# Kernel tuning notes

Measured on AMD Instinct MI355X. Metric: run time of the kernel, lower is better.

The kernel has to match this reference:

```python
import jax, jax.numpy as jnp
import numpy as np

K = 32        # num_classes
NQ = 16384    # num query samples
C = 512       # feature_dim
H_REF = 512   # refinement_net hidden
H_CONF = 256  # confidence_net hidden
NUM_STEPS = 3


def setup_inputs() -> dict:
    key = jax.random.key(0)
    ks = jax.random.split(key, 8)
    s = 0.02
    return {
        "prototypes": jax.random.normal(ks[0], (K, C), jnp.float32),
        "query_features": jax.random.normal(ks[1], (NQ, C), jnp.float32),
        "query_distances": jax.random.uniform(ks[2], (NQ, K), jnp.float32) * 10.0,
        "W1": jax.random.normal(ks[3], (2 * C, H_REF), jnp.float32) * s,
        "b1": jnp.zeros((H_REF,), jnp.float32),
        "W2": jax.random.normal(ks[4], (H_REF, C), jnp.float32) * s,
        "b2": jnp.zeros((C,), jnp.float32),
        "Wc1": jax.random.normal(ks[5], (2 * C, H_CONF), jnp.float32) * s,
        "bc1": jnp.zeros((H_CONF,), jnp.float32),
        "Wc2": jax.random.normal(ks[6], (H_CONF, 1), jnp.float32) * s,
        "bc2": jnp.zeros((1,), jnp.float32),
    }


def reference(prototypes, query_features, query_distances,
              W1, b1, W2, b2, Wc1, bc1, Wc2, bc2):
    # ---- refinement loop (3 steps, sequential in refined prototypes) ----
    refined = prototypes
    for step in range(NUM_STEPS):
        # soft assignments over classes; temperature = step + 1
        soft = jax.nn.softmax(-query_distances / (step + 1.0), axis=-1)  # (NQ, K)
        wsum = jnp.maximum(soft.sum(axis=0), 1e-6)                       # (K,)  clamp(min=1e-6)
        wmean = (soft.T @ query_features) / wsum[:, None]                # (K, C)
        concat = jnp.concatenate([refined, wmean], axis=-1)              # (K, 2C)
        h = jax.nn.relu(concat @ W1 + b1)                                # dropout is identity in eval
        refinement = h @ W2 + b2                                         # (K, C)
        refined = refined + 0.1 * refinement

    # ---- confidence scores: MLP on [proto, query] pairs, mean over queries ----
    # Split first-layer weight into proto half and query half to avoid
    # materializing the (K, NQ, 2C) concat explicitly (same math).
    Wp, Wq = Wc1[:C], Wc1[C:]
    hp = prototypes @ Wp          # (K, H_CONF)
    hq = query_features @ Wq      # (NQ, H_CONF)
    hidden = jax.nn.relu(hp[:, None, :] + hq[None, :, :] + bc1)  # (K, NQ, H_CONF)
    conf = jax.nn.sigmoid(hidden @ Wc2 + bc2)                    # (K, NQ, 1)
    confidence_scores = conf.reshape(K, -1).mean(axis=1)         # (K,)

    return refined, confidence_scores
```

## Files before the change

### kernel.cpp

```cpp
#include <hip/hip_runtime.h>

#define NQg 16384

typedef __attribute__((ext_vector_type(8))) short short8;
typedef __attribute__((ext_vector_type(4))) short short4_t;
typedef __attribute__((ext_vector_type(8))) __bf16 bf16x8;
typedef __attribute__((ext_vector_type(4))) float floatx4;

union S8B8 { short8 s; bf16x8 b; };

__device__ __forceinline__ short f2bf(float f) {
    union { float f; unsigned u; } v; v.f = f;
    unsigned r = v.u + 0x7fffu + ((v.u >> 16) & 1u);
    return (short)(r >> 16);
}
__device__ __forceinline__ float bf2f(short s) {
    union { unsigned u; float f; } v; v.u = ((unsigned)(unsigned short)s) << 16;
    return v.f;
}
__device__ __forceinline__ float bflo(unsigned u) { return __uint_as_float(u << 16); }
__device__ __forceinline__ float bfhi(unsigned u) { return __uint_as_float(u & 0xffff0000u); }

__global__ __launch_bounds__(256) void k_A(const float* __restrict__ qd,
                                           const float* __restrict__ W1, const float* __restrict__ W2,
                                           const float* __restrict__ Wc1, const float* __restrict__ proto,
                                           const float* __restrict__ qf, const float* __restrict__ bc1,
                                           short* __restrict__ softT,
                                           short* __restrict__ W1p, short* __restrict__ W2p,
                                           short* __restrict__ wqp, float* __restrict__ refined,
                                           short* __restrict__ qf2b, float* __restrict__ wmean,
                                           float* __restrict__ hpb,
                                           int* __restrict__ bar, float* __restrict__ dout) {
    int tid = threadIdx.x, bid = blockIdx.x;
    if (bid < 64) {
        int q = bid * 256 + tid;
        float d[32];
        const float4* p = (const float4*)(qd + (size_t)q * 32);
#pragma unroll
        for (int j = 0; j < 8; j++) {
            float4 v = p[j];
            d[4 * j] = v.x; d[4 * j + 1] = v.y; d[4 * j + 2] = v.z; d[4 * j + 3] = v.w;
        }
#pragma unroll
        for (int s = 0; s < 3; s++) {
            float inv = -1.0f / (float)(s + 1);
            float e[32];
            float sum = 0.f;
#pragma unroll
            for (int k = 0; k < 32; k++) { e[k] = __expf(d[k] * inv); sum += e[k]; }
            float r = 1.0f / sum;
#pragma unroll
            for (int k = 0; k < 32; k++)
                softT[(size_t)(s * 32 + k) * NQg + q] = f2bf(e[k] * r);
        }
        return;
    }
    if (bid < 512) {
        int idx = (bid - 64) * 256 + tid;
        if (idx < 65536) {
            int kg = idx >> 9, n = idx & 511;
            short8 o;
#pragma unroll
            for (int j = 0; j < 8; j++) o[j] = f2bf(W1[(size_t)(kg * 8 + j) * 512 + n]);
            *(short8*)&W1p[((size_t)kg * 512 + n) * 8] = o;
        } else if (idx < 98304) {
            int j2 = idx - 65536;
            int kg = j2 >> 9, n = j2 & 511;
            short8 o;
#pragma unroll
            for (int j = 0; j < 8; j++) o[j] = f2bf(W2[(size_t)(kg * 8 + j) * 512 + n]);
            *(short8*)&W2p[((size_t)kg * 512 + n) * 8] = o;
        } else {
            int j3 = idx - 98304;
            int kg = j3 >> 8, n = j3 & 255;
            short8 o;
#pragma unroll
            for (int j = 0; j < 8; j++) o[j] = f2bf(Wc1[(size_t)(512 + kg * 8 + j) * 256 + n]);
            *(short8*)&wqp[((size_t)kg * 256 + n) * 8] = o;
        }
        return;
    }
    if (bid < 576) {
        int idx = (bid - 512) * 256 + tid;
        refined[idx] = proto[idx];
        return;
    }
    if (bid < 768) {
        int idx = (bid - 576) * 256 + tid;
        wmean[idx] = 0.f;
        return;
    }
    if (bid < 2816) {
#pragma unroll
        for (int it = 0; it < 4; it++) {
            int j = (bid - 768) * 1024 + it * 256 + tid;
            float4 v = *(const float4*)&qf[(size_t)j * 4];
            short4_t o;
            o[0] = f2bf(v.x); o[1] = f2bf(v.y); o[2] = f2bf(v.z); o[3] = f2bf(v.w);
            *(short4_t*)&qf2b[(size_t)j * 4] = o;
        }
        return;
    }
    if (bid < 2848) {
        int r = bid - 2816;
        const float* pr = proto + r * 512;
        const float* wc = Wc1 + tid;
        float a0 = 0.f, a1 = 0.f, a2 = 0.f, a3 = 0.f;
#pragma unroll 4
        for (int i = 0; i < 512; i += 4) {
            float4 p4 = *(const float4*)&pr[i];
            float w0 = wc[(size_t)i * 256];
            float w1 = wc[(size_t)(i + 1) * 256];
            float w2 = wc[(size_t)(i + 2) * 256];
            float w3 = wc[(size_t)(i + 3) * 256];
            a0 += p4.x * w0;
            a1 += p4.y * w1;
            a2 += p4.z * w2;
            a3 += p4.w * w3;
        }
        hpb[r * 256 + tid] = bc1[tid] + ((a0 + a1) + (a2 + a3));
        return;
    }
    {
        if (tid < 8) bar[tid] = 0;
        else if (tid >= 32 && tid < 64) dout[16384 + tid - 32] = 0.f;
    }
}

__global__ __launch_bounds__(256) void k_B(const short* __restrict__ qf2b,
                                           const short* __restrict__ softT,
                                           float* __restrict__ wmean,
                                           float* __restrict__ wsuminv,
                                           const short* __restrict__ wqp,
                                           const float* __restrict__ hpb,
                                           const float* __restrict__ Wc2,
                                           const float* __restrict__ bc2p,
                                           float* __restrict__ dout) {
    __shared__ float smem[6688];
    int tid = threadIdx.x;
    int lane = tid & 63, w = tid >> 6;
    int ml = lane & 15, q8 = lane >> 4;
    int bid = blockIdx.x;

    if (bid < 256) {
        short* B_lds = (short*)smem;
        int kc = bid >> 2, ns = bid & 3;
        int c0 = ns * 128;
        int qbase0 = kc * 256;
        int c_l = 2 * lane;
        int q_l = 8 * w;

        floatx4 acc[6][2];
#pragma unroll
        for (int mt = 0; mt < 6; mt++)
#pragma unroll
            for (int nt = 0; nt < 2; nt++) acc[mt][nt] = (floatx4){0.f, 0.f, 0.f, 0.f};

        for (int step = 0; step < 8; step++) {
            int qb = qbase0 + step * 32;
            short8 sA, sB;
#pragma unroll
            for (int i = 0; i < 8; i++) {
                unsigned u = *(const unsigned*)&qf2b[(size_t)(qb + q_l + i) * 512 + c0 + c_l];
                sA[i] = (short)(u & 0xffffu);
                sB[i] = (short)(u >> 16);
            }
            __syncthreads();
            *(short8*)&B_lds[c_l * 40 + q_l] = sA;
            *(short8*)&B_lds[(c_l + 1) * 40 + q_l] = sB;
            S8B8 a[6];
#pragma unroll
            for (int mt = 0; mt < 6; mt++)
                a[mt].s = *(const short8*)&softT[(size_t)(mt * 16 + ml) * NQg + qb + q8 * 8];
            __syncthreads();
#pragma unroll
            for (int nt = 0; nt < 2; nt++) {
                S8B8 b; b.s = *(short8*)&B_lds[(w * 32 + nt * 16 + ml) * 40 + q8 * 8];
#pragma unroll
                for (int mt = 0; mt < 6; mt++)
                    acc[mt][nt] = __builtin_amdgcn_mfma_f32_16x16x32_bf16(a[mt].b, b.b, acc[mt][nt], 0, 0, 0);
            }
        }
        int mrot = kc % 6;
#pragma unroll
        for (int mtt = 0; mtt < 6; mtt++) {
            int mt = mtt + mrot; if (mt >= 6) mt -= 6;
#pragma unroll
            for (int nt = 0; nt < 2; nt++) {
                int c = c0 + w * 32 + nt * 16 + ml;
#pragma unroll
                for (int r = 0; r < 4; r++) {
                    int m = mt * 16 + q8 * 4 + r;
                    atomicAdd(&wmean[(size_t)m * 512 + c], acc[mt][nt][r]);
                }
            }
        }
    } else if (bid < 352) {
        float* red = smem;
        int sk = bid - 256;
        const short* row = softT + (size_t)sk * NQg;
        float s = 0.f;
#pragma unroll
        for (int j = 0; j < 8; j++) {
            short8 v = *(const short8*)&row[j * 2048 + tid * 8];
#pragma unroll
            for (int i = 0; i < 8; i++) s += bf2f(v[i]);
        }
        red[tid] = s;
        __syncthreads();
        for (int off = 128; off > 0; off >>= 1) {
            if (tid < off) red[tid] += red[tid + off];
            __syncthreads();
        }
        if (tid == 0) wsuminv[sk] = 1.0f / fmaxf(red[0], 1e-6f);
    } else {
        short* hq_lds = (short*)smem;
        short* hp_s   = (short*)smem + 4480;
        float* wc2s   = smem + 6400;
        float* confl  = smem + 6656;
        int q0 = (bid - 352) * 16;

        wc2s[tid] = Wc2[tid];
        if (tid < 32) confl[tid] = 0.f;
#pragma unroll
        for (int i = 0; i < 8; i++) {
            int idx = i * 256 + tid;
            int r = idx >> 6, c = (idx & 63) * 4;
            float4 v = *(const float4*)&hpb[r * 256 + c];
            short4_t o;
            o[0] = f2bf(v.x); o[1] = f2bf(v.y); o[2] = f2bf(v.z); o[3] = f2bf(v.w);
            *(short4_t*)&hp_s[r * 260 + c] = o;
        }
        {
            floatx4 acc[4];
#pragma unroll
            for (int nt = 0; nt < 4; nt++) acc[nt] = (floatx4){0.f, 0.f, 0.f, 0.f};
            const short* qa = qf2b + (size_t)(q0 + ml) * 512 + q8 * 8;
#pragma unroll 4
            for (int kc = 0; kc < 512; kc += 32) {
                S8B8 a; a.s = *(const short8*)&qa[kc];
#pragma unroll
                for (int nt = 0; nt < 4; nt++) {
                    int col = w * 64 + nt * 16 + ml;
                    S8B8 b; b.s = *(const short8*)&wqp[((size_t)((kc >> 3) + q8) * 256 + col) * 8];
                    acc[nt] = __builtin_amdgcn_mfma_f32_16x16x32_bf16(a.b, b.b, acc[nt], 0, 0, 0);
                }
            }
#pragma unroll
            for (int nt = 0; nt < 4; nt++)
#pragma unroll
                for (int r = 0; r < 4; r++)
                    hq_lds[(q8 * 4 + r) * 280 + w * 64 + nt * 16 + ml] = f2bf(acc[nt][r]);
        }
        __syncthreads();

        int q = tid & 15, kg = tid >> 4;
        int k0 = kg, k1 = kg + 16;
        float s0 = 0.f, s1 = 0.f;
        for (int h = 0; h < 256; h += 4) {
            uint2 hv = *(uint2*)&hq_lds[q * 280 + h];
            float f0 = bflo(hv.x), f1 = bfhi(hv.x), f2 = bflo(hv.y), f3 = bfhi(hv.y);
            uint2 u0 = *(uint2*)&hp_s[k0 * 260 + h];
            uint2 u1 = *(uint2*)&hp_s[k1 * 260 + h];
            float4 wv = *(float4*)&wc2s[h];
            s0 += fmaxf(bflo(u0.x) + f0, 0.f) * wv.x;
            s0 += fmaxf(bfhi(u0.x) + f1, 0.f) * wv.y;
            s0 += fmaxf(bflo(u0.y) + f2, 0.f) * wv.z;
            s0 += fmaxf(bfhi(u0.y) + f3, 0.f) * wv.w;
            s1 += fmaxf(bflo(u1.x) + f0, 0.f) * wv.x;
            s1 += fmaxf(bfhi(u1.x) + f1, 0.f) * wv.y;
            s1 += fmaxf(bflo(u1.y) + f2, 0.f) * wv.z;
            s1 += fmaxf(bfhi(u1.y) + f3, 0.f) * wv.w;
        }
        float bc2 = bc2p[0];
        float v0 = 1.f / (1.f + __expf(-(s0 + bc2)));
        float v1 = 1.f / (1.f + __expf(-(s1 + bc2)));
        atomicAdd(&confl[k0], v0);
        atomicAdd(&confl[k1], v1);
        __syncthreads();
        if (tid < 32) {
            int cell = (tid + bid) & 31;
            atomicAdd(&dout[16384 + cell], confl[cell] * (1.0f / 16384.0f));
        }
    }
}

__device__ __forceinline__ void gbar(int* bar, int phase, int nblk) {
    __syncthreads();
    if (threadIdx.x == 0) {
        __threadfence();
        __hip_atomic_fetch_add(&bar[phase], 1, __ATOMIC_ACQ_REL, __HIP_MEMORY_SCOPE_AGENT);
        while (__hip_atomic_load(&bar[phase], __ATOMIC_ACQUIRE, __HIP_MEMORY_SCOPE_AGENT) < nblk)
            __builtin_amdgcn_s_sleep(1);
    }
    __syncthreads();
}

__global__ __launch_bounds__(256) void k_D(const float* __restrict__ wmean,
                                           const float* __restrict__ wsuminv,
                                           const short* __restrict__ W1p,
                                           const float* __restrict__ b1,
                                           const short* __restrict__ W2p,
                                           const float* __restrict__ b2,
                                           float* __restrict__ refined,
                                           short* __restrict__ hb,
                                           int* __restrict__ bar,
                                           float* __restrict__ dout) {
    __shared__ float smem[4608];
    int tid = threadIdx.x, lane = tid & 63, w = tid >> 6;
    int ml = lane & 15, q8 = lane >> 4;

    float (*red)[32][36] = (float(*)[32][36])smem;
    int nb = blockIdx.x;
    int phase = 0;
    for (int s = 0; s < 3; s++) {
        {
            const float* srcA = (w < 2) ? refined : (wmean + (size_t)s * 32 * 512 - 512);
            float iv0 = 1.f, iv1 = 1.f;
            if (w >= 2) {
                iv0 = wsuminv[s * 32 + ml];
                iv1 = wsuminv[s * 32 + 16 + ml];
            }
            int kw = w * 256;
            floatx4 acc[2][2];
#pragma unroll
            for (int mt = 0; mt < 2; mt++)
#pragma unroll
                for (int nt = 0; nt < 2; nt++) acc[mt][nt] = (floatx4){0.f, 0.f, 0.f, 0.f};
            for (int st = 0; st < 8; st++) {
                int k0 = kw + st * 32 + q8 * 8;
                S8B8 a[2];
#pragma unroll
                for (int mt = 0; mt < 2; mt++) {
                    float sc = mt ? iv1 : iv0;
                    const float* p = &srcA[(size_t)(mt * 16 + ml) * 512 + k0];
                    float4 f0 = *(const float4*)p;
                    float4 f1 = *(const float4*)(p + 4);
                    short8 t;
                    t[0] = f2bf(f0.x * sc); t[1] = f2bf(f0.y * sc);
                    t[2] = f2bf(f0.z * sc); t[3] = f2bf(f0.w * sc);
                    t[4] = f2bf(f1.x * sc); t[5] = f2bf(f1.y * sc);
                    t[6] = f2bf(f1.z * sc); t[7] = f2bf(f1.w * sc);
                    a[mt].s = t;
                }
#pragma unroll
                for (int nt = 0; nt < 2; nt++) {
                    int n = nb * 32 + nt * 16 + ml;
                    S8B8 b; b.s = *(const short8*)&W1p[((size_t)(k0 >> 3) * 512 + n) * 8];
#pragma unroll
                    for (int mt = 0; mt < 2; mt++)
                        acc[mt][nt] = __builtin_amdgcn_mfma_f32_16x16x32_bf16(a[mt].b, b.b, acc[mt][nt], 0, 0, 0);
                }
            }
            __syncthreads();
#pragma unroll
            for (int mt = 0; mt < 2; mt++)
#pragma unroll
                for (int nt = 0; nt < 2; nt++)
#pragma unroll
                    for (int r = 0; r < 4; r++)
                        red[w][mt * 16 + q8 * 4 + r][nt * 16 + ml] = acc[mt][nt][r];
            __syncthreads();
            int m = tid >> 3, n0 = (tid & 7) * 4;
            short4_t o;
#pragma unroll
            for (int i = 0; i < 4; i++) {
                float v = b1[nb * 32 + n0 + i];
#pragma unroll
                for (int w4 = 0; w4 < 4; w4++) v += red[w4][m][n0 + i];
                o[i] = f2bf(fmaxf(v, 0.f));
            }
            *(short4_t*)&hb[(size_t)m * 512 + nb * 32 + n0] = o;
        }
        gbar(bar, phase++, 16);
        {
            int kw = w * 128;
            floatx4 acc[2][2];
#pragma unroll
            for (int mt = 0; mt < 2; mt++)
#pragma unroll
                for (int nt = 0; nt < 2; nt++) acc[mt][nt] = (floatx4){0.f, 0.f, 0.f, 0.f};
            for (int st = 0; st < 4; st++) {
                int k0 = kw + st * 32 + q8 * 8;
                S8B8 a[2];
#pragma unroll
                for (int mt = 0; mt < 2; mt++)
                    a[mt].s = *(const short8*)&hb[(size_t)(mt * 16 + ml) * 512 + k0];
#pragma unroll
                for (int nt = 0; nt < 2; nt++) {
                    int n = nb * 32 + nt * 16 + ml;
                    S8B8 b; b.s = *(const short8*)&W2p[((size_t)(k0 >> 3) * 512 + n) * 8];
#pragma unroll
                    for (int mt = 0; mt < 2; mt++)
                        acc[mt][nt] = __builtin_amdgcn_mfma_f32_16x16x32_bf16(a[mt].b, b.b, acc[mt][nt], 0, 0, 0);
                }
            }
            __syncthreads();
#pragma unroll
            for (int mt = 0; mt < 2; mt++)
#pragma unroll
                for (int nt = 0; nt < 2; nt++)
#pragma unroll
                    for (int r = 0; r < 4; r++)
                        red[w][mt * 16 + q8 * 4 + r][nt * 16 + ml] = acc[mt][nt][r];
            __syncthreads();
            int m = tid >> 3, n0 = (tid & 7) * 4;
#pragma unroll
            for (int i = 0; i < 4; i++) {
                int c = nb * 32 + n0 + i;
                float v = b2[c];
#pragma unroll
                for (int w4 = 0; w4 < 4; w4++) v += red[w4][m][n0 + i];
                float val = refined[(size_t)m * 512 + c] + 0.1f * v;
                refined[(size_t)m * 512 + c] = val;
                if (s == 2) dout[(size_t)m * 512 + c] = val;
            }
        }
        if (s < 2) gbar(bar, phase++, 16);
    }
}

extern "C" void kernel_launch(void* const* d_in, const int* in_sizes, int n_in,
                              void* d_out, int out_size, void* d_ws, size_t ws_size,
                              hipStream_t stream) {
    const float* proto = (const float*)d_in[0];
    const float* qf    = (const float*)d_in[1];
    const float* qd    = (const float*)d_in[2];
    const float* W1    = (const float*)d_in[3];
    const float* b1    = (const float*)d_in[4];
    const float* W2    = (const float*)d_in[5];
    const float* b2    = (const float*)d_in[6];
    const float* Wc1   = (const float*)d_in[7];
    const float* bc1   = (const float*)d_in[8];
    const float* Wc2   = (const float*)d_in[9];
    const float* bc2   = (const float*)d_in[10];
    float* out = (float*)d_out;

    float* ws = (float*)d_ws;
    short* softT   = (short*)ws;
    short* qf2b    = (short*)(ws + 786432);
    float* wmean   = ws + 4980736;
    float* refined = ws + 5029888;
    short* hb      = (short*)(ws + 5046272);
    short* W1p     = (short*)(ws + 5054464);
    short* W2p     = (short*)(ws + 5316608);
    short* wqp     = (short*)(ws + 5447680);
    float* hpb     = ws + 5513216;
    int*   bar     = (int*)(ws + 5521408);
    float* wsuminv = ws + 5521416;

    k_A<<<2849, 256, 0, stream>>>(qd, W1, W2, Wc1, proto, qf, bc1, softT, W1p, W2p, wqp,
                                  refined, qf2b, wmean, hpb, bar, out);
    k_B<<<1376, 256, 0, stream>>>(qf2b, softT, wmean, wsuminv, wqp, hpb, Wc2, bc2, out);
    k_D<<<16, 256, 0, stream>>>(wmean, wsuminv, W1p, b1, W2p, b2, refined, hb, bar, out);
}
```

Baseline: 200.7 us.

## Overlap serial refinement loop with confidence MLP and batch hq GEMM

Moves the confidence pair-MLP blocks out of k_B and into the same launch as the 16-block serial refinement loop, which now runs at raised priority. The idea is to hide the latency-bound refinement chain behind the parallel confidence work. The hq = qf@Wq projection now runs as its own 64x64-tiled GEMM in k_B and is staged through a global bf16 buffer, so per-16-row blocks no longer redo the weight loads. The wmean split doubles its block count, which means twice as many atomics. There is some risk that the spin-wait barrier blocks get starved or interleave badly with the other blocks.

```diff
diff --git a/kernel.cpp b/kernel.cpp
--- a/kernel.cpp
+++ b/kernel.cpp
@@ -129,96 +129,267 @@
 
 __global__ __launch_bounds__(256) void k_B(const short* __restrict__ qf2b,
                                            const short* __restrict__ softT,
+                                           const short* __restrict__ wqp,
                                            float* __restrict__ wmean,
-                                           float* __restrict__ wsuminv,
-                                           const short* __restrict__ wqp,
+                                           short* __restrict__ hq_g,
+                                           float* __restrict__ wsuminv) {
+    __shared__ short B_lds[128 * 40];
+    int tid = threadIdx.x;
+    int lane = tid & 63, w = tid >> 6;
+    int ml = lane & 15, q8 = lane >> 4;
+
+    if (blockIdx.x < 512) {
+        int kc = blockIdx.x >> 2, ns = blockIdx.x & 3;
+        int c0 = ns * 128;
+        int qbase0 = kc * 128;
+        int c_l = 2 * lane;
+        int q_l = 8 * w;
+
+        floatx4 acc[6][2];
+#pragma unroll
+        for (int mt = 0; mt < 6; mt++)
+#pragma unroll
+            for (int nt = 0; nt < 2; nt++) acc[mt][nt] = (floatx4){0.f, 0.f, 0.f, 0.f};
+
+        for (int step = 0; step < 4; step++) {
+            int qb = qbase0 + step * 32;
+            short8 sA, sB;
+#pragma unroll
+            for (int i = 0; i < 8; i++) {
+                unsigned u = *(const unsigned*)&qf2b[(size_t)(qb + q_l + i) * 512 + c0 + c_l];
+                sA[i] = (short)(u & 0xffffu);
+                sB[i] = (short)(u >> 16);
+            }
+            __syncthreads();
+            *(short8*)&B_lds[c_l * 40 + q_l] = sA;
+            *(short8*)&B_lds[(c_l + 1) * 40 + q_l] = sB;
+            S8B8 a[6];
+#pragma unroll
+            for (int mt = 0; mt < 6; mt++)
+                a[mt].s = *(const short8*)&softT[(size_t)(mt * 16 + ml) * NQg + qb + q8 * 8];
+            __syncthreads();
+#pragma unroll
+            for (int nt = 0; nt < 2; nt++) {
+                S8B8 b; b.s = *(short8*)&B_lds[(w * 32 + nt * 16 + ml) * 40 + q8 * 8];
+#pragma unroll
+                for (int mt = 0; mt < 6; mt++)
+                    acc[mt][nt] = __builtin_amdgcn_mfma_f32_16x16x32_bf16(a[mt].b, b.b, acc[mt][nt], 0, 0, 0);
+            }
+        }
+#pragma unroll
+        for (int mt = 0; mt < 6; mt++) {
+#pragma unroll
+            for (int nt = 0; nt < 2; nt++) {
+                int c = c0 + w * 32 + nt * 16 + ml;
+#pragma unroll
+                for (int r = 0; r < 4; r++) {
+                    int m = mt * 16 + q8 * 4 + r;
+                    atomicAdd(&wmean[(size_t)m * 512 + c], acc[mt][nt][r]);
+                }
+            }
+        }
+    } else if (blockIdx.x < 768) {
+        int m0 = (blockIdx.x - 512) * 64;
+        int n0 = w * 64;
+        floatx4 acc[4][4];
+#pragma unroll
+        for (int mt = 0; mt < 4; mt++)
+#pragma unroll
+            for (int nt = 0; nt < 4; nt++) acc[mt][nt] = (floatx4){0.f, 0.f, 0.f, 0.f};
+
+#pragma unroll 4
+        for (int kc = 0; kc < 512; kc += 32) {
+            S8B8 a[4], b[4];
+#pragma unroll
+            for (int mt = 0; mt < 4; mt++)
+                a[mt].s = *(const short8*)&qf2b[(size_t)(m0 + mt * 16 + ml) * 512 + kc + q8 * 8];
+#pragma unroll
+            for (int nt = 0; nt < 4; nt++)
+                b[nt].s = *(const short8*)&wqp[((size_t)((kc >> 3) + q8) * 256 + n0 + nt * 16 + ml) * 8];
+#pragma unroll
+            for (int mt = 0; mt < 4; mt++)
+#pragma unroll
+                for (int nt = 0; nt < 4; nt++)
+                    acc[mt][nt] = __builtin_amdgcn_mfma_f32_16x16x32_bf16(a[mt].b, b[nt].b, acc[mt][nt], 0, 0, 0);
+        }
+#pragma unroll
+        for (int mt = 0; mt < 4; mt++)
+#pragma unroll
+            for (int nt = 0; nt < 4; nt++) {
+                int col = n0 + nt * 16 + ml;
+#pragma unroll
+                for (int r = 0; r < 4; r++) {
+                    int row = m0 + mt * 16 + q8 * 4 + r;
+                    hq_g[(size_t)row * 256 + col] = f2bf(acc[mt][nt][r]);
+                }
+            }
+    } else {
+        float* red = (float*)B_lds;
+        int sk = blockIdx.x - 768;
+        const short* row = softT + (size_t)sk * NQg;
+        float s = 0.f;
+#pragma unroll
+        for (int j = 0; j < 8; j++) {
+            short8 v = *(const short8*)&row[j * 2048 + tid * 8];
+#pragma unroll
+            for (int i = 0; i < 8; i++) s += bf2f(v[i]);
+        }
+        red[tid] = s;
+        __syncthreads();
+        for (int off = 128; off > 0; off >>= 1) {
+            if (tid < off) red[tid] += red[tid + off];
+            __syncthreads();
+        }
+        if (tid == 0) wsuminv[sk] = 1.0f / fmaxf(red[0], 1e-6f);
+    }
+}
+
+__device__ __forceinline__ void gbar(int* bar, int phase, int nblk) {
+    __syncthreads();
+    if (threadIdx.x == 0) {
+        __threadfence();
+        __hip_atomic_fetch_add(&bar[phase], 1, __ATOMIC_ACQ_REL, __HIP_MEMORY_SCOPE_AGENT);
+        while (__hip_atomic_load(&bar[phase], __ATOMIC_ACQUIRE, __HIP_MEMORY_SCOPE_AGENT) < nblk)
+            __builtin_amdgcn_s_sleep(1);
+    }
+    __syncthreads();
+}
+
+__global__ __launch_bounds__(256) void k_D(const float* __restrict__ wmean,
+                                           const float* __restrict__ wsuminv,
+                                           const short* __restrict__ W1p,
+                                           const float* __restrict__ b1,
+                                           const short* __restrict__ W2p,
+                                           const float* __restrict__ b2,
+                                           float* __restrict__ refined,
+                                           short* __restrict__ hb,
+                                           int* __restrict__ bar,
+                                           const short* __restrict__ hq_g,
                                            const float* __restrict__ hpb,
                                            const float* __restrict__ Wc2,
                                            const float* __restrict__ bc2p,
                                            float* __restrict__ dout) {
     __shared__ float smem[6688];
-    int tid = threadIdx.x;
-    int lane = tid & 63, w = tid >> 6;
+    int tid = threadIdx.x, lane = tid & 63, w = tid >> 6;
     int ml = lane & 15, q8 = lane >> 4;
-    int bid = blockIdx.x;
-
-    if (bid < 256) {
-        short* B_lds = (short*)smem;
-        int kc = bid >> 2, ns = bid & 3;
-        int c0 = ns * 128;
-        int qbase0 = kc * 256;
-        int c_l = 2 * lane;
-        int q_l = 8 * w;
-
-        floatx4 acc[6][2];
-#pragma unroll
-        for (int mt = 0; mt < 6; mt++)
-#pragma unroll
-            for (int nt = 0; nt < 2; nt++) acc[mt][nt] = (floatx4){0.f, 0.f, 0.f, 0.f};
-
-        for (int step = 0; step < 8; step++) {
-            int qb = qbase0 + step * 32;
-            short8 sA, sB;
-#pragma unroll
-            for (int i = 0; i < 8; i++) {
-                unsigned u = *(const unsigned*)&qf2b[(size_t)(qb + q_l + i) * 512 + c0 + c_l];
-                sA[i] = (short)(u & 0xffffu);
-                sB[i] = (short)(u >> 16);
-            }
-            __syncthreads();
-            *(short8*)&B_lds[c_l * 40 + q_l] = sA;
-            *(short8*)&B_lds[(c_l + 1) * 40 + q_l] = sB;
-            S8B8 a[6];
-#pragma unroll
-            for (int mt = 0; mt < 6; mt++)
-                a[mt].s = *(const short8*)&softT[(size_t)(mt * 16 + ml) * NQg + qb + q8 * 8];
-            __syncthreads();
-#pragma unroll
-            for (int nt = 0; nt < 2; nt++) {
-                S8B8 b; b.s = *(short8*)&B_lds[(w * 32 + nt * 16 + ml) * 40 + q8 * 8];
-#pragma unroll
-                for (int mt = 0; mt < 6; mt++)
-                    acc[mt][nt] = __builtin_amdgcn_mfma_f32_16x16x32_bf16(a[mt].b, b.b, acc[mt][nt], 0, 0, 0);
-            }
-        }
-        int mrot = kc % 6;
-#pragma unroll
-        for (int mtt = 0; mtt < 6; mtt++) {
-            int mt = mtt + mrot; if (mt >= 6) mt -= 6;
-#pragma unroll
-            for (int nt = 0; nt < 2; nt++) {
-                int c = c0 + w * 32 + nt * 16 + ml;
-#pragma unroll
-                for (int r = 0; r < 4; r++) {
-                    int m = mt * 16 + q8 * 4 + r;
-                    atomicAdd(&wmean[(size_t)m * 512 + c], acc[mt][nt][r]);
-                }
-            }
-        }
-    } else if (bid < 352) {
-        float* red = smem;
-        int sk = bid - 256;
-        const short* row = softT + (size_t)sk * NQg;
-        float s = 0.f;
-#pragma unroll
-        for (int j = 0; j < 8; j++) {
-            short8 v = *(const short8*)&row[j * 2048 + tid * 8];
-#pragma unroll
-            for (int i = 0; i < 8; i++) s += bf2f(v[i]);
-        }
-        red[tid] = s;
-        __syncthreads();
-        for (int off = 128; off > 0; off >>= 1) {
-            if (tid < off) red[tid] += red[tid + off];
-            __syncthreads();
-        }
-        if (tid == 0) wsuminv[sk] = 1.0f / fmaxf(red[0], 1e-6f);
+
+    if (blockIdx.x < 16) {
+        __builtin_amdgcn_s_setprio(1);
+        float (*red)[32][36] = (float(*)[32][36])smem;
+        int nb = blockIdx.x;
+        int phase = 0;
+        for (int s = 0; s < 3; s++) {
+            {
+                const float* srcA = (w < 2) ? refined : (wmean + (size_t)s * 32 * 512 - 512);
+                float iv0 = 1.f, iv1 = 1.f;
+                if (w >= 2) {
+                    iv0 = wsuminv[s * 32 + ml];
+                    iv1 = wsuminv[s * 32 + 16 + ml];
+                }
+                int kw = w * 256;
+                floatx4 acc[2][2];
+#pragma unroll
+                for (int mt = 0; mt < 2; mt++)
+#pragma unroll
+                    for (int nt = 0; nt < 2; nt++) acc[mt][nt] = (floatx4){0.f, 0.f, 0.f, 0.f};
+                for (int st = 0; st < 8; st++) {
+                    int k0 = kw + st * 32 + q8 * 8;
+                    S8B8 a[2];
+#pragma unroll
+                    for (int mt = 0; mt < 2; mt++) {
+                        float sc = mt ? iv1 : iv0;
+                        const float* p = &srcA[(size_t)(mt * 16 + ml) * 512 + k0];
+                        float4 f0 = *(const float4*)p;
+                        float4 f1 = *(const float4*)(p + 4);
+                        short8 t;
+                        t[0] = f2bf(f0.x * sc); t[1] = f2bf(f0.y * sc);
+                        t[2] = f2bf(f0.z * sc); t[3] = f2bf(f0.w * sc);
+                        t[4] = f2bf(f1.x * sc); t[5] = f2bf(f1.y * sc);
+                        t[6] = f2bf(f1.z * sc); t[7] = f2bf(f1.w * sc);
+                        a[mt].s = t;
+                    }
+#pragma unroll
+                    for (int nt = 0; nt < 2; nt++) {
+                        int n = nb * 32 + nt * 16 + ml;
+                        S8B8 b; b.s = *(const short8*)&W1p[((size_t)(k0 >> 3) * 512 + n) * 8];
+#pragma unroll
+                        for (int mt = 0; mt < 2; mt++)
+                            acc[mt][nt] = __builtin_amdgcn_mfma_f32_16x16x32_bf16(a[mt].b, b.b, acc[mt][nt], 0, 0, 0);
+                    }
+                }
+                __syncthreads();
+#pragma unroll
+                for (int mt = 0; mt < 2; mt++)
+#pragma unroll
+                    for (int nt = 0; nt < 2; nt++)
+#pragma unroll
+                        for (int r = 0; r < 4; r++)
+                            red[w][mt * 16 + q8 * 4 + r][nt * 16 + ml] = acc[mt][nt][r];
+                __syncthreads();
+                int m = tid >> 3, n0 = (tid & 7) * 4;
+                short4_t o;
+#pragma unroll
+                for (int i = 0; i < 4; i++) {
+                    float v = b1[nb * 32 + n0 + i];
+#pragma unroll
+                    for (int w4 = 0; w4 < 4; w4++) v += red[w4][m][n0 + i];
+                    o[i] = f2bf(fmaxf(v, 0.f));
+                }
+                *(short4_t*)&hb[(size_t)m * 512 + nb * 32 + n0] = o;
+            }
+            gbar(bar, phase++, 16);
+            {
+                int kw = w * 128;
+                floatx4 acc[2][2];
+#pragma unroll
+                for (int mt = 0; mt < 2; mt++)
+#pragma unroll
+                    for (int nt = 0; nt < 2; nt++) acc[mt][nt] = (floatx4){0.f, 0.f, 0.f, 0.f};
+                for (int st = 0; st < 4; st++) {
+                    int k0 = kw + st * 32 + q8 * 8;
+                    S8B8 a[2];
+#pragma unroll
+                    for (int mt = 0; mt < 2; mt++)
+                        a[mt].s = *(const short8*)&hb[(size_t)(mt * 16 + ml) * 512 + k0];
+#pragma unroll
+                    for (int nt = 0; nt < 2; nt++) {
+                        int n = nb * 32 + nt * 16 + ml;
+                        S8B8 b; b.s = *(const short8*)&W2p[((size_t)(k0 >> 3) * 512 + n) * 8];
+#pragma unroll
+                        for (int mt = 0; mt < 2; mt++)
+                            acc[mt][nt] = __builtin_amdgcn_mfma_f32_16x16x32_bf16(a[mt].b, b.b, acc[mt][nt], 0, 0, 0);
+                    }
+                }
+                __syncthreads();
+#pragma unroll
+                for (int mt = 0; mt < 2; mt++)
+#pragma unroll
+                    for (int nt = 0; nt < 2; nt++)
+#pragma unroll
+                        for (int r = 0; r < 4; r++)
+                            red[w][mt * 16 + q8 * 4 + r][nt * 16 + ml] = acc[mt][nt][r];
+                __syncthreads();
+                int m = tid >> 3, n0 = (tid & 7) * 4;
+#pragma unroll
+                for (int i = 0; i < 4; i++) {
+                    int c = nb * 32 + n0 + i;
+                    float v = b2[c];
+#pragma unroll
+                    for (int w4 = 0; w4 < 4; w4++) v += red[w4][m][n0 + i];
+                    float val = refined[(size_t)m * 512 + c] + 0.1f * v;
+                    refined[(size_t)m * 512 + c] = val;
+                    if (s == 2) dout[(size_t)m * 512 + c] = val;
+                }
+            }
+            if (s < 2) gbar(bar, phase++, 16);
+        }
+        __builtin_amdgcn_s_setprio(0);
     } else {
         short* hq_lds = (short*)smem;
         short* hp_s   = (short*)smem + 4480;
         float* wc2s   = smem + 6400;
         float* confl  = smem + 6656;
-        int q0 = (bid - 352) * 16;
+        int q0 = (blockIdx.x - 16) * 16;
 
         wc2s[tid] = Wc2[tid];
         if (tid < 32) confl[tid] = 0.f;
@@ -232,25 +403,10 @@
             *(short4_t*)&hp_s[r * 260 + c] = o;
         }
         {
-            floatx4 acc[4];
-#pragma unroll
-            for (int nt = 0; nt < 4; nt++) acc[nt] = (floatx4){0.f, 0.f, 0.f, 0.f};
-            const short* qa = qf2b + (size_t)(q0 + ml) * 512 + q8 * 8;
-#pragma unroll 4
-            for (int kc = 0; kc < 512; kc += 32) {
-                S8B8 a; a.s = *(const short8*)&qa[kc];
-#pragma unroll
-                for (int nt = 0; nt < 4; nt++) {
-                    int col = w * 64 + nt * 16 + ml;
-                    S8B8 b; b.s = *(const short8*)&wqp[((size_t)((kc >> 3) + q8) * 256 + col) * 8];
-                    acc[nt] = __builtin_amdgcn_mfma_f32_16x16x32_bf16(a.b, b.b, acc[nt], 0, 0, 0);
-                }
-            }
-#pragma unroll
-            for (int nt = 0; nt < 4; nt++)
-#pragma unroll
-                for (int r = 0; r < 4; r++)
-                    hq_lds[(q8 * 4 + r) * 280 + w * 64 + nt * 16 + ml] = f2bf(acc[nt][r]);
+            const short* hqs = hq_g + (size_t)q0 * 256;
+            int r = tid >> 4, c = (tid & 15) * 16;
+            *(short8*)&hq_lds[r * 280 + c] = *(const short8*)&hqs[r * 256 + c];
+            *(short8*)&hq_lds[r * 280 + c + 8] = *(const short8*)&hqs[r * 256 + c + 8];
         }
         __syncthreads();
 
@@ -279,144 +435,9 @@
         atomicAdd(&confl[k1], v1);
         __syncthreads();
         if (tid < 32) {
-            int cell = (tid + bid) & 31;
+            int cell = (tid + blockIdx.x) & 31;
             atomicAdd(&dout[16384 + cell], confl[cell] * (1.0f / 16384.0f));
         }
-    }
-}
-
-__device__ __forceinline__ void gbar(int* bar, int phase, int nblk) {
-    __syncthreads();
-    if (threadIdx.x == 0) {
-        __threadfence();
-        __hip_atomic_fetch_add(&bar[phase], 1, __ATOMIC_ACQ_REL, __HIP_MEMORY_SCOPE_AGENT);
-        while (__hip_atomic_load(&bar[phase], __ATOMIC_ACQUIRE, __HIP_MEMORY_SCOPE_AGENT) < nblk)
-            __builtin_amdgcn_s_sleep(1);
-    }
-    __syncthreads();
-}
-
-__global__ __launch_bounds__(256) void k_D(const float* __restrict__ wmean,
-                                           const float* __restrict__ wsuminv,
-                                           const short* __restrict__ W1p,
-                                           const float* __restrict__ b1,
-                                           const short* __restrict__ W2p,
-                                           const float* __restrict__ b2,
-                                           float* __restrict__ refined,
-                                           short* __restrict__ hb,
-                                           int* __restrict__ bar,
-                                           float* __restrict__ dout) {
-    __shared__ float smem[4608];
-    int tid = threadIdx.x, lane = tid & 63, w = tid >> 6;
-    int ml = lane & 15, q8 = lane >> 4;
-
-    float (*red)[32][36] = (float(*)[32][36])smem;
-    int nb = blockIdx.x;
-    int phase = 0;
-    for (int s = 0; s < 3; s++) {
-        {
-            const float* srcA = (w < 2) ? refined : (wmean + (size_t)s * 32 * 512 - 512);
-            float iv0 = 1.f, iv1 = 1.f;
-            if (w >= 2) {
-                iv0 = wsuminv[s * 32 + ml];
-                iv1 = wsuminv[s * 32 + 16 + ml];
-            }
-            int kw = w * 256;
-            floatx4 acc[2][2];
-#pragma unroll
-            for (int mt = 0; mt < 2; mt++)
-#pragma unroll
-                for (int nt = 0; nt < 2; nt++) acc[mt][nt] = (floatx4){0.f, 0.f, 0.f, 0.f};
-            for (int st = 0; st < 8; st++) {
-                int k0 = kw + st * 32 + q8 * 8;
-                S8B8 a[2];
-#pragma unroll
-                for (int mt = 0; mt < 2; mt++) {
-                    float sc = mt ? iv1 : iv0;
-                    const float* p = &srcA[(size_t)(mt * 16 + ml) * 512 + k0];
-                    float4 f0 = *(const float4*)p;
-                    float4 f1 = *(const float4*)(p + 4);
-                    short8 t;
-                    t[0] = f2bf(f0.x * sc); t[1] = f2bf(f0.y * sc);
-                    t[2] = f2bf(f0.z * sc); t[3] = f2bf(f0.w * sc);
-                    t[4] = f2bf(f1.x * sc); t[5] = f2bf(f1.y * sc);
-                    t[6] = f2bf(f1.z * sc); t[7] = f2bf(f1.w * sc);
-                    a[mt].s = t;
-                }
-#pragma unroll
-                for (int nt = 0; nt < 2; nt++) {
-                    int n = nb * 32 + nt * 16 + ml;
-                    S8B8 b; b.s = *(const short8*)&W1p[((size_t)(k0 >> 3) * 512 + n) * 8];
-#pragma unroll
-                    for (int mt = 0; mt < 2; mt++)
-                        acc[mt][nt] = __builtin_amdgcn_mfma_f32_16x16x32_bf16(a[mt].b, b.b, acc[mt][nt], 0, 0, 0);
-                }
-            }
-            __syncthreads();
-#pragma unroll
-            for (int mt = 0; mt < 2; mt++)
-#pragma unroll
-                for (int nt = 0; nt < 2; nt++)
-#pragma unroll
-                    for (int r = 0; r < 4; r++)
-                        red[w][mt * 16 + q8 * 4 + r][nt * 16 + ml] = acc[mt][nt][r];
-            __syncthreads();
-            int m = tid >> 3, n0 = (tid & 7) * 4;
-            short4_t o;
-#pragma unroll
-            for (int i = 0; i < 4; i++) {
-                float v = b1[nb * 32 + n0 + i];
-#pragma unroll
-                for (int w4 = 0; w4 < 4; w4++) v += red[w4][m][n0 + i];
-                o[i] = f2bf(fmaxf(v, 0.f));
-            }
-            *(short4_t*)&hb[(size_t)m * 512 + nb * 32 + n0] = o;
-        }
-        gbar(bar, phase++, 16);
-        {
-            int kw = w * 128;
-            floatx4 acc[2][2];
-#pragma unroll
-            for (int mt = 0; mt < 2; mt++)
-#pragma unroll
-                for (int nt = 0; nt < 2; nt++) acc[mt][nt] = (floatx4){0.f, 0.f, 0.f, 0.f};
-            for (int st = 0; st < 4; st++) {
-                int k0 = kw + st * 32 + q8 * 8;
-                S8B8 a[2];
-#pragma unroll
-                for (int mt = 0; mt < 2; mt++)
-                    a[mt].s = *(const short8*)&hb[(size_t)(mt * 16 + ml) * 512 + k0];
-#pragma unroll
-                for (int nt = 0; nt < 2; nt++) {
-                    int n = nb * 32 + nt * 16 + ml;
-                    S8B8 b; b.s = *(const short8*)&W2p[((size_t)(k0 >> 3) * 512 + n) * 8];
-#pragma unroll
-                    for (int mt = 0; mt < 2; mt++)
-                        acc[mt][nt] = __builtin_amdgcn_mfma_f32_16x16x32_bf16(a[mt].b, b.b, acc[mt][nt], 0, 0, 0);
-                }
-            }
-            __syncthreads();
-#pragma unroll
-            for (int mt = 0; mt < 2; mt++)
-#pragma unroll
-                for (int nt = 0; nt < 2; nt++)
-#pragma unroll
-                    for (int r = 0; r < 4; r++)
-                        red[w][mt * 16 + q8 * 4 + r][nt * 16 + ml] = acc[mt][nt][r];
-            __syncthreads();
-            int m = tid >> 3, n0 = (tid & 7) * 4;
-#pragma unroll
-            for (int i = 0; i < 4; i++) {
-                int c = nb * 32 + n0 + i;
-                float v = b2[c];
-#pragma unroll
-                for (int w4 = 0; w4 < 4; w4++) v += red[w4][m][n0 + i];
-                float val = refined[(size_t)m * 512 + c] + 0.1f * v;
-                refined[(size_t)m * 512 + c] = val;
-                if (s == 2) dout[(size_t)m * 512 + c] = val;
-            }
-        }
-        if (s < 2) gbar(bar, phase++, 16);
     }
 }
 
@@ -448,9 +469,11 @@
     float* hpb     = ws + 5513216;
     int*   bar     = (int*)(ws + 5521408);
     float* wsuminv = ws + 5521416;
+    short* hq      = (short*)(ws + 5521536);
 
     k_A<<<2849, 256, 0, stream>>>(qd, W1, W2, Wc1, proto, qf, bc1, softT, W1p, W2p, wqp,
                                   refined, qf2b, wmean, hpb, bar, out);
-    k_B<<<1376, 256, 0, stream>>>(qf2b, softT, wmean, wsuminv, wqp, hpb, Wc2, bc2, out);
-    k_D<<<16, 256, 0, stream>>>(wmean, wsuminv, W1p, b1, W2p, b2, refined, hb, bar, out);
-}
+    k_B<<<864, 256, 0, stream>>>(qf2b, softT, wqp, wmean, hq, wsuminv);
+    k_D<<<1040, 256, 0, stream>>>(wmean, wsuminv, W1p, b1, W2p, b2, refined, hb, bar,
+                                  hq, hpb, Wc2, bc2, out);
+}
```

After: 189.8 us. -5.4%, faster.
